# Kernel optimization log

Hardware: AMD Instinct MI355X
Metric: run time of the kernel (lower is better)

The kernel has to match this reference:

```python
import jax, jax.numpy as jnp
import numpy as np

G, N, E, F_IN, F_OUT, C = 256, 512, 4096, 64, 64, 16


def setup_inputs() -> dict:
    key = jax.random.key(0)
    ks = jax.random.split(key, 6)
    x_batch = jax.random.normal(ks[0], (G, N, F_IN), dtype=jnp.float32)
    edge_index_batch = jax.random.randint(ks[1], (G, 2, E), 0, N, dtype=jnp.int32)
    conv_weight = jax.random.normal(ks[2], (F_OUT, F_IN), dtype=jnp.float32) * (1.0 / np.sqrt(F_IN))
    conv_bias = jax.random.normal(ks[3], (F_OUT,), dtype=jnp.float32) * 0.02
    lin_weight = jax.random.normal(ks[4], (C, F_OUT * N), dtype=jnp.float32) * (1.0 / np.sqrt(F_OUT * N))
    lin_bias = jax.random.normal(ks[5], (C,), dtype=jnp.float32) * 0.02
    return {"x_batch": x_batch, "edge_index_batch": edge_index_batch,
            "conv_weight": conv_weight, "conv_bias": conv_bias,
            "lin_weight": lin_weight, "lin_bias": lin_bias}


def _gcn_conv_graph(xw, edge_index, self_loops):
    # xw: [N, F_OUT] (already linearly transformed), edge_index: [2, E]
    row = jnp.concatenate([edge_index[0], self_loops])  # sources
    col = jnp.concatenate([edge_index[1], self_loops])  # targets
    ones = jnp.ones(row.shape[0], dtype=xw.dtype)
    deg = jax.ops.segment_sum(ones, col, num_segments=N)  # degree at target nodes
    dinv = jnp.where(deg > 0, jax.lax.rsqrt(deg), jnp.zeros_like(deg))
    norm = dinv[row] * dinv[col]                          # [E+N]
    msgs = xw[row] * norm[:, None]                        # gather + normalize
    return jax.ops.segment_sum(msgs, col, num_segments=N)  # scatter-add at targets


def reference(x_batch, edge_index_batch, conv_weight, conv_bias, lin_weight, lin_bias):
    # GCNConv (PyG defaults: self-loops, symmetric normalization, post-agg bias)
    xw = jnp.einsum('gnf,of->gno', x_batch, conv_weight)  # [G, N, F_OUT]
    self_loops = jnp.arange(N, dtype=edge_index_batch.dtype)
    h = jax.vmap(_gcn_conv_graph, in_axes=(0, 0, None))(xw, edge_index_batch, self_loops)
    h = h + conv_bias
    h = jax.nn.relu(h)
    flat = h.reshape(h.shape[0], -1)                      # [G, N*F_OUT]
    logits = flat @ lin_weight.T + lin_bias               # [G, C]
    return jax.nn.log_softmax(logits, axis=-1)
```

## Files before the change

kernel.cpp:

```cpp
#include <hip/hip_runtime.h>

#define Gn 256
#define Nn 512
#define En 4096
#define Fn 64
#define Cn 16
#define ET (En + Nn)

typedef _Float16 halfv8 __attribute__((ext_vector_type(8)));
typedef _Float16 halfv4 __attribute__((ext_vector_type(4)));
typedef float    f32x4  __attribute__((ext_vector_type(4)));

__device__ __forceinline__ float pk_norm(unsigned p) {
    return (float)__builtin_bit_cast(_Float16, (unsigned short)(p & 0xffffu));
}

__global__ __launch_bounds__(1024, 4) void gcn_agg_conv(
    const float* __restrict__ x,
    const int*   __restrict__ ei,
    const float* __restrict__ w,
    const float* __restrict__ wbias,
    _Float16* __restrict__ hout)
{
    __shared__ unsigned short xs_h[Nn * Fn];
    __shared__ unsigned short xhs[Nn * Fn];
    __shared__ unsigned short wts[Fn * Fn];
    __shared__ unsigned int   epk[ET + 8];
    __shared__ float dinv[Nn];
    __shared__ int   cnt[Nn];
    __shared__ int   wsum[8];

    const int g    = blockIdx.x;
    const int tid  = threadIdx.x;
    const int lane = tid & 63;
    const int wid  = tid >> 6;

    const float* xg = x + (size_t)g * Nn * Fn;
    const int*   es = ei + (size_t)g * 2 * En;
    const int*   ed = es + En;

    if (tid < Nn) dinv[tid] = 1.0f;
    __syncthreads();

    for (int e = tid; e < En; e += 1024) atomicAdd(&dinv[ed[e]], 1.0f);
    #pragma unroll
    for (int it = 0; it < 8; ++it) {
        int idx = tid + it * 1024;
        float4 v = *(const float4*)(xg + idx * 4);
        halfv4 hv; hv[0]=(_Float16)v.x; hv[1]=(_Float16)v.y;
                   hv[2]=(_Float16)v.z; hv[3]=(_Float16)v.w;
        *(halfv4*)((char*)xs_h + idx * 8) = hv;
    }
    {
        int o = tid >> 4, f0 = (tid & 15) * 4;
        float4 v = *(const float4*)(w + o * Fn + f0);
        halfv4 hv; hv[0]=(_Float16)v.x; hv[1]=(_Float16)v.y;
                   hv[2]=(_Float16)v.z; hv[3]=(_Float16)v.w;
        int blk = f0 >> 3, hf = (f0 >> 2) & 1;
        *(halfv4*)((char*)wts + o * 128 + ((blk ^ (o & 7)) * 16) + hf * 8) = hv;
    }
    __syncthreads();

    int c = 0;
    if (tid < Nn) { float d = dinv[tid]; c = (int)d; dinv[tid] = rsqrtf(d); }
    int v_ = c;
    #pragma unroll
    for (int off = 1; off < 64; off <<= 1) {
        int u = __shfl_up(v_, off, 64);
        if (lane >= off) v_ += u;
    }
    if (wid < 8 && lane == 63) wsum[wid] = v_;
    __syncthreads();
    if (tid == 0) { int a = 0; for (int i = 0; i < 8; ++i) { int t = wsum[i]; wsum[i] = a; a += t; } }
    __syncthreads();
    if (tid < Nn) cnt[tid] = v_ - c + wsum[wid];
    __syncthreads();

    for (int e = tid; e < ET; e += 1024) {
        int s, t;
        if (e < En) { s = es[e]; t = ed[e]; } else { s = e - En; t = s; }
        float nrm = dinv[s] * dinv[t];
        int slot = atomicAdd(&cnt[t], 1);
        unsigned short nb = __builtin_bit_cast(unsigned short, (_Float16)nrm);
        epk[slot] = ((unsigned)s << 16) | nb;
    }
    __syncthreads();

    {
        const int qid = lane >> 4, fl = lane & 15;
        for (int r = 0; r < 8; ++r) {
            int t = r * 64 + wid * 4 + qid;
            int beg = (t == 0) ? 0 : cnt[t - 1];
            int end = cnt[t];
            float a0 = 0.f, a1 = 0.f, a2 = 0.f, a3 = 0.f;
            unsigned pA0 = epk[beg],     pA1 = epk[beg + 1];
            unsigned pA2 = epk[beg + 2], pA3 = epk[beg + 3];
            int j = beg;
            for (; j + 4 <= end; j += 4) {
                unsigned pB0 = epk[j + 4], pB1 = epk[j + 5];
                unsigned pB2 = epk[j + 6], pB3 = epk[j + 7];
                int s0 = pA0 >> 16, s1 = pA1 >> 16, s2 = pA2 >> 16, s3 = pA3 >> 16;
                float n0 = pk_norm(pA0), n1 = pk_norm(pA1);
                float n2 = pk_norm(pA2), n3 = pk_norm(pA3);
                halfv4 x0 = *(const halfv4*)((const char*)xs_h + s0 * 128 + fl * 8);
                halfv4 x1 = *(const halfv4*)((const char*)xs_h + s1 * 128 + fl * 8);
                halfv4 x2 = *(const halfv4*)((const char*)xs_h + s2 * 128 + fl * 8);
                halfv4 x3 = *(const halfv4*)((const char*)xs_h + s3 * 128 + fl * 8);
                a0 += n0 * (float)x0[0] + n1 * (float)x1[0] + n2 * (float)x2[0] + n3 * (float)x3[0];
                a1 += n0 * (float)x0[1] + n1 * (float)x1[1] + n2 * (float)x2[1] + n3 * (float)x3[1];
                a2 += n0 * (float)x0[2] + n1 * (float)x1[2] + n2 * (float)x2[2] + n3 * (float)x3[2];
                a3 += n0 * (float)x0[3] + n1 * (float)x1[3] + n2 * (float)x2[3] + n3 * (float)x3[3];
                pA0 = pB0; pA1 = pB1; pA2 = pB2; pA3 = pB3;
            }
            for (; j < end; ++j) {
                int s = pA0 >> 16;
                float nm = pk_norm(pA0);
                halfv4 xv = *(const halfv4*)((const char*)xs_h + s * 128 + fl * 8);
                a0 += nm * (float)xv[0]; a1 += nm * (float)xv[1];
                a2 += nm * (float)xv[2]; a3 += nm * (float)xv[3];
                pA0 = pA1; pA1 = pA2; pA2 = pA3;
            }
            halfv4 hv; hv[0]=(_Float16)a0; hv[1]=(_Float16)a1;
                       hv[2]=(_Float16)a2; hv[3]=(_Float16)a3;
            int dw = t * 32 + (((fl >> 1) ^ (t & 7)) * 4) + (fl & 1) * 2;
            *(halfv4*)((char*)xhs + dw * 4) = hv;
        }
    }
    __syncthreads();

    {
        const int m = lane & 15, q = lane >> 4;
        #pragma unroll
        for (int j = 0; j < 8; ++j) {
            int idx = wid * 8 + j, tm = idx >> 2, to = idx & 3;
            int n = tm * 16 + m, o = to * 16 + m;
            halfv8 X0 = *(const halfv8*)((const char*)xhs + n * 128 + ((q       ^ (n & 7)) * 16));
            halfv8 X1 = *(const halfv8*)((const char*)xhs + n * 128 + (((4 + q) ^ (n & 7)) * 16));
            halfv8 W0 = *(const halfv8*)((const char*)wts + o * 128 + ((q       ^ (o & 7)) * 16));
            halfv8 W1 = *(const halfv8*)((const char*)wts + o * 128 + (((4 + q) ^ (o & 7)) * 16));
            f32x4 acc = {0.f, 0.f, 0.f, 0.f};
            acc = __builtin_amdgcn_mfma_f32_16x16x32_f16(W0, X0, acc, 0, 0, 0);
            acc = __builtin_amdgcn_mfma_f32_16x16x32_f16(W1, X1, acc, 0, 0, 0);
            float4 bq = *(const float4*)&wbias[to * 16 + q * 4];
            halfv4 hv;
            hv[0] = (_Float16)fmaxf(acc[0] + bq.x, 0.0f);
            hv[1] = (_Float16)fmaxf(acc[1] + bq.y, 0.0f);
            hv[2] = (_Float16)fmaxf(acc[2] + bq.z, 0.0f);
            hv[3] = (_Float16)fmaxf(acc[3] + bq.w, 0.0f);
            int sw = (to * 4 + q) ^ m;
            *(halfv4*)((char*)xs_h + n * 128 + sw * 8) = hv;
        }
    }
    __syncthreads();

    {
        _Float16* hg = hout + (size_t)g * (Nn * Fn);
        #pragma unroll
        for (int it = 0; it < 8; ++it) {
            int i = tid + it * 1024;
            int n = i >> 4, g64 = i & 15;
            uint2 vv = *(const uint2*)((const char*)xs_h + (n * 16 + (g64 ^ (n & 15))) * 8);
            *(uint2*)((char*)hg + (size_t)i * 8) = vv;
        }
    }
}

__global__ __launch_bounds__(256) void gcn_linear(
    const _Float16* __restrict__ h,
    const float* __restrict__ lw,
    float* __restrict__ part)
{
    __shared__ float red[4][64][4];
    const int cx = blockIdx.x;
    const int gy = blockIdx.y;
    const int tid = threadIdx.x, lane = tid & 63, wid = tid >> 6;
    const int ml = lane & 15, q = lane >> 4;

    const size_t kbase = (size_t)cx * 1024 + wid * 256;
    const _Float16* ha = h  + (size_t)(gy * 16 + ml) * (Nn * Fn) + kbase + q * 8;
    const float*    lb = lw + (size_t)ml * (Nn * Fn) + kbase + q * 8;

    f32x4 acc = {0.f, 0.f, 0.f, 0.f};
    #pragma unroll
    for (int ks = 0; ks < 8; ++ks) {
        halfv8 a = *(const halfv8*)(ha + ks * 32);
        float4 b0 = *(const float4*)(lb + ks * 32);
        float4 b1 = *(const float4*)(lb + ks * 32 + 4);
        halfv8 b; b[0]=(_Float16)b0.x; b[1]=(_Float16)b0.y; b[2]=(_Float16)b0.z;
                  b[3]=(_Float16)b0.w; b[4]=(_Float16)b1.x; b[5]=(_Float16)b1.y;
                  b[6]=(_Float16)b1.z; b[7]=(_Float16)b1.w;
        acc = __builtin_amdgcn_mfma_f32_16x16x32_f16(a, b, acc, 0, 0, 0);
    }
    #pragma unroll
    for (int r = 0; r < 4; ++r) red[wid][lane][r] = acc[r];
    __syncthreads();
    {
        int m = tid >> 4, cc = tid & 15;
        int sl = (m >> 2) * 16 + cc, rg = m & 3;
        float v = red[0][sl][rg] + red[1][sl][rg] + red[2][sl][rg] + red[3][sl][rg];
        part[(((size_t)(gy * 16 + m)) * 32 + cx) * Cn + cc] = v;
    }
}

__global__ __launch_bounds__(64) void gcn_softmax(
    const float* __restrict__ part,
    const float* __restrict__ lbias,
    float* __restrict__ out)
{
    const int g = blockIdx.x, lane = threadIdx.x;
    if (lane < Cn) {
        float v = lbias[lane];
        #pragma unroll
        for (int s = 0; s < 32; ++s) v += part[((size_t)g * 32 + s) * Cn + lane];
        float m = v;
        #pragma unroll
        for (int off = 8; off > 0; off >>= 1) m = fmaxf(m, __shfl_xor(m, off, 16));
        float ex = expf(v - m);
        float ssum = ex;
        #pragma unroll
        for (int off = 8; off > 0; off >>= 1) ssum += __shfl_xor(ssum, off, 16);
        out[g * Cn + lane] = v - m - logf(ssum);
    }
}

extern "C" void kernel_launch(void* const* d_in, const int* in_sizes, int n_in,
                              void* d_out, int out_size, void* d_ws, size_t ws_size,
                              hipStream_t stream) {
    const float* x  = (const float*)d_in[0];
    const int*   ei = (const int*)d_in[1];
    const float* w  = (const float*)d_in[2];
    const float* wb = (const float*)d_in[3];
    const float* lw = (const float*)d_in[4];
    const float* lb = (const float*)d_in[5];
    float* out = (float*)d_out;

    _Float16* hbuf = (_Float16*)d_ws;
    float* part = (float*)((char*)d_ws + (size_t)Gn * Nn * Fn * 2);

    hipLaunchKernelGGL(gcn_agg_conv, dim3(Gn), dim3(1024), 0, stream,
                       x, ei, w, wb, hbuf);
    hipLaunchKernelGGL(gcn_linear, dim3(32, 16), dim3(256), 0, stream,
                       hbuf, lw, part);
    hipLaunchKernelGGL(gcn_softmax, dim3(Gn), dim3(64), 0, stream,
                       part, lb, out);
}
```

Baseline: 113.4 us.

## Split fused GCN kernel into conversion, CSR build, half-graph aggregation and linear kernels

Replaces the single per-graph aggregation kernel with separate kernels. One converts x to fp16 in global memory, one converts and permutes the linear weight to fp16, one builds the CSR edge list per graph, and one aggregates half a graph per block with gathers read from global memory instead of LDS. The hidden layer is written in a tiled layout matched to the permuted linear weights, and the linear kernel now loads fp16 weights directly. The aim is more blocks per graph, less LDS per block for higher occupancy, and no repeated weight conversion. In exchange it adds extra launches and global round trips for the converted x and the CSR arrays.

```diff
diff --git a/kernel.cpp b/kernel.cpp
--- a/kernel.cpp
+++ b/kernel.cpp
@@ -6,6 +6,7 @@
 #define Fn 64
 #define Cn 16
 #define ET (En + Nn)
+#define EPAD 4616
 
 typedef _Float16 halfv8 __attribute__((ext_vector_type(8)));
 typedef _Float16 halfv4 __attribute__((ext_vector_type(4)));
@@ -15,97 +16,141 @@
     return (float)__builtin_bit_cast(_Float16, (unsigned short)(p & 0xffffu));
 }
 
-__global__ __launch_bounds__(1024, 4) void gcn_agg_conv(
-    const float* __restrict__ x,
-    const int*   __restrict__ ei,
-    const float* __restrict__ w,
-    const float* __restrict__ wbias,
+__global__ __launch_bounds__(256) void cvt_x(const float* __restrict__ x,
+                                             _Float16* __restrict__ xc) {
+    size_t base = (size_t)blockIdx.x * 256 + threadIdx.x;
+    #pragma unroll
+    for (int it = 0; it < 4; ++it) {
+        size_t i = base + (size_t)it * (2048 * 256);
+        float4 v = ((const float4*)x)[i];
+        halfv4 h; h[0]=(_Float16)v.x; h[1]=(_Float16)v.y;
+                  h[2]=(_Float16)v.z; h[3]=(_Float16)v.w;
+        ((halfv4*)xc)[i] = h;
+    }
+}
+
+__global__ __launch_bounds__(256) void cvt_lw_perm(const float* __restrict__ lw,
+                                                   _Float16* __restrict__ lwh) {
+    int u = blockIdx.x * 256 + threadIdx.x;
+    int c = u >> 13, v = u & 8191;
+    int jobidx = v >> 6, q = (v >> 4) & 3, m = v & 15;
+    int n = (jobidx >> 2) * 16 + m;
+    int o = (jobidx & 3) * 16 + q * 4;
+    float4 f = *(const float4*)(lw + (size_t)c * (Nn * Fn) + n * 64 + o);
+    halfv4 h; h[0]=(_Float16)f.x; h[1]=(_Float16)f.y;
+              h[2]=(_Float16)f.z; h[3]=(_Float16)f.w;
+    *(halfv4*)(lwh + (size_t)c * (Nn * Fn) + (size_t)v * 4) = h;
+}
+
+__global__ __launch_bounds__(256) void build_csr(const int* __restrict__ ei,
+                                                 unsigned* __restrict__ epkG,
+                                                 int* __restrict__ cntG) {
+    __shared__ int      degL[Nn];
+    __shared__ float    dinvL[Nn];
+    __shared__ int      cntE[Nn];
+    __shared__ unsigned epkL[ET];
+    __shared__ int      wsum[4];
+    const int g = blockIdx.x, tid = threadIdx.x;
+    const int lane = tid & 63, wid = tid >> 6;
+    const int* es = ei + (size_t)g * 2 * En;
+    const int* ed = es + En;
+
+    degL[tid] = 0; degL[tid + 256] = 0;
+    __syncthreads();
+    for (int e = tid; e < En; e += 256) atomicAdd(&degL[ed[e]], 1);
+    __syncthreads();
+
+    const int t2 = tid * 2;
+    int cA = degL[t2] + 1, cB = degL[t2 + 1] + 1;
+    dinvL[t2]     = rsqrtf((float)cA);
+    dinvL[t2 + 1] = rsqrtf((float)cB);
+    int p = cA + cB, v = p;
+    #pragma unroll
+    for (int off = 1; off < 64; off <<= 1) {
+        int u = __shfl_up(v, off, 64);
+        if (lane >= off) v += u;
+    }
+    if (lane == 63) wsum[wid] = v;
+    __syncthreads();
+    if (tid == 0) { int a = 0; for (int i = 0; i < 4; ++i) { int t = wsum[i]; wsum[i] = a; a += t; } }
+    __syncthreads();
+    int pe = v - p + wsum[wid];
+    cntE[t2] = pe;
+    cntE[t2 + 1] = pe + cA;
+    __syncthreads();
+
+    for (int e = tid; e < ET; e += 256) {
+        int s, t;
+        if (e < En) { s = es[e]; t = ed[e]; } else { s = t = e - En; }
+        float nrm = dinvL[s] * dinvL[t];
+        int slot = atomicAdd(&cntE[t], 1);
+        unsigned short nb = __builtin_bit_cast(unsigned short, (_Float16)nrm);
+        epkL[slot] = ((unsigned)s << 16) | nb;
+    }
+    __syncthreads();
+
+    for (int i = tid; i < ET; i += 256) epkG[(size_t)g * EPAD + i] = epkL[i];
+    cntG[(size_t)g * Nn + t2]     = cntE[t2];
+    cntG[(size_t)g * Nn + t2 + 1] = cntE[t2 + 1];
+}
+
+__global__ __launch_bounds__(512, 4) void agg_conv(
+    const _Float16* __restrict__ xc,
+    const unsigned* __restrict__ epkG,
+    const int*      __restrict__ cntG,
+    const float*    __restrict__ w,
+    const float*    __restrict__ wbias,
     _Float16* __restrict__ hout)
 {
-    __shared__ unsigned short xs_h[Nn * Fn];
-    __shared__ unsigned short xhs[Nn * Fn];
+    __shared__ unsigned short xhs[256 * Fn];
     __shared__ unsigned short wts[Fn * Fn];
-    __shared__ unsigned int   epk[ET + 8];
-    __shared__ float dinv[Nn];
-    __shared__ int   cnt[Nn];
-    __shared__ int   wsum[8];
-
-    const int g    = blockIdx.x;
-    const int tid  = threadIdx.x;
-    const int lane = tid & 63;
-    const int wid  = tid >> 6;
-
-    const float* xg = x + (size_t)g * Nn * Fn;
-    const int*   es = ei + (size_t)g * 2 * En;
-    const int*   ed = es + En;
-
-    if (tid < Nn) dinv[tid] = 1.0f;
-    __syncthreads();
-
-    for (int e = tid; e < En; e += 1024) atomicAdd(&dinv[ed[e]], 1.0f);
-    #pragma unroll
-    for (int it = 0; it < 8; ++it) {
-        int idx = tid + it * 1024;
-        float4 v = *(const float4*)(xg + idx * 4);
-        halfv4 hv; hv[0]=(_Float16)v.x; hv[1]=(_Float16)v.y;
-                   hv[2]=(_Float16)v.z; hv[3]=(_Float16)v.w;
-        *(halfv4*)((char*)xs_h + idx * 8) = hv;
-    }
-    {
-        int o = tid >> 4, f0 = (tid & 15) * 4;
-        float4 v = *(const float4*)(w + o * Fn + f0);
-        halfv4 hv; hv[0]=(_Float16)v.x; hv[1]=(_Float16)v.y;
-                   hv[2]=(_Float16)v.z; hv[3]=(_Float16)v.w;
-        int blk = f0 >> 3, hf = (f0 >> 2) & 1;
-        *(halfv4*)((char*)wts + o * 128 + ((blk ^ (o & 7)) * 16) + hf * 8) = hv;
-    }
-    __syncthreads();
-
-    int c = 0;
-    if (tid < Nn) { float d = dinv[tid]; c = (int)d; dinv[tid] = rsqrtf(d); }
-    int v_ = c;
-    #pragma unroll
-    for (int off = 1; off < 64; off <<= 1) {
-        int u = __shfl_up(v_, off, 64);
-        if (lane >= off) v_ += u;
-    }
-    if (wid < 8 && lane == 63) wsum[wid] = v_;
-    __syncthreads();
-    if (tid == 0) { int a = 0; for (int i = 0; i < 8; ++i) { int t = wsum[i]; wsum[i] = a; a += t; } }
-    __syncthreads();
-    if (tid < Nn) cnt[tid] = v_ - c + wsum[wid];
-    __syncthreads();
-
-    for (int e = tid; e < ET; e += 1024) {
-        int s, t;
-        if (e < En) { s = es[e]; t = ed[e]; } else { s = e - En; t = s; }
-        float nrm = dinv[s] * dinv[t];
-        int slot = atomicAdd(&cnt[t], 1);
-        unsigned short nb = __builtin_bit_cast(unsigned short, (_Float16)nrm);
-        epk[slot] = ((unsigned)s << 16) | nb;
-    }
-    __syncthreads();
-
-    {
+    __shared__ unsigned epkL[ET + 16];
+    __shared__ int cntl[260];
+    const int hh = blockIdx.x, g = blockIdx.y;
+    const int tid = threadIdx.x, lane = tid & 63, wid = tid >> 6;
+    const int tbase = hh * 256;
+
+    const int slotlo = (hh == 0) ? 0 : cntG[(size_t)g * Nn + tbase - 1];
+    const int slothi = cntG[(size_t)g * Nn + tbase + 255];
+    const int total  = slothi - slotlo;
+
+    if (tid < 257)
+        cntl[tid] = (tid == 0) ? slotlo : cntG[(size_t)g * Nn + tbase + tid - 1];
+    for (int i = tid; i < total; i += 512)
+        epkL[i] = epkG[(size_t)g * EPAD + slotlo + i];
+    {
+        int o = tid >> 3, b8 = tid & 7;
+        float4 va = *(const float4*)(w + o * Fn + b8 * 8);
+        float4 vb = *(const float4*)(w + o * Fn + b8 * 8 + 4);
+        halfv8 hv; hv[0]=(_Float16)va.x; hv[1]=(_Float16)va.y;
+                   hv[2]=(_Float16)va.z; hv[3]=(_Float16)va.w;
+                   hv[4]=(_Float16)vb.x; hv[5]=(_Float16)vb.y;
+                   hv[6]=(_Float16)vb.z; hv[7]=(_Float16)vb.w;
+        *(halfv8*)((char*)wts + o * 128 + ((b8 ^ (o & 7)) * 16)) = hv;
+    }
+    __syncthreads();
+
+    {
+        const _Float16* xgc = xc + (size_t)g * (Nn * Fn);
         const int qid = lane >> 4, fl = lane & 15;
         for (int r = 0; r < 8; ++r) {
-            int t = r * 64 + wid * 4 + qid;
-            int beg = (t == 0) ? 0 : cnt[t - 1];
-            int end = cnt[t];
+            int tl = r * 32 + wid * 4 + qid;
+            int beg = cntl[tl] - slotlo;
+            int end = cntl[tl + 1] - slotlo;
             float a0 = 0.f, a1 = 0.f, a2 = 0.f, a3 = 0.f;
-            unsigned pA0 = epk[beg],     pA1 = epk[beg + 1];
-            unsigned pA2 = epk[beg + 2], pA3 = epk[beg + 3];
+            unsigned pA0 = epkL[beg],     pA1 = epkL[beg + 1];
+            unsigned pA2 = epkL[beg + 2], pA3 = epkL[beg + 3];
             int j = beg;
             for (; j + 4 <= end; j += 4) {
-                unsigned pB0 = epk[j + 4], pB1 = epk[j + 5];
-                unsigned pB2 = epk[j + 6], pB3 = epk[j + 7];
+                unsigned pB0 = epkL[j + 4], pB1 = epkL[j + 5];
+                unsigned pB2 = epkL[j + 6], pB3 = epkL[j + 7];
                 int s0 = pA0 >> 16, s1 = pA1 >> 16, s2 = pA2 >> 16, s3 = pA3 >> 16;
                 float n0 = pk_norm(pA0), n1 = pk_norm(pA1);
                 float n2 = pk_norm(pA2), n3 = pk_norm(pA3);
-                halfv4 x0 = *(const halfv4*)((const char*)xs_h + s0 * 128 + fl * 8);
-                halfv4 x1 = *(const halfv4*)((const char*)xs_h + s1 * 128 + fl * 8);
-                halfv4 x2 = *(const halfv4*)((const char*)xs_h + s2 * 128 + fl * 8);
-                halfv4 x3 = *(const halfv4*)((const char*)xs_h + s3 * 128 + fl * 8);
+                halfv4 x0 = *(const halfv4*)(xgc + s0 * Fn + fl * 4);
+                halfv4 x1 = *(const halfv4*)(xgc + s1 * Fn + fl * 4);
+                halfv4 x2 = *(const halfv4*)(xgc + s2 * Fn + fl * 4);
+                halfv4 x3 = *(const halfv4*)(xgc + s3 * Fn + fl * 4);
                 a0 += n0 * (float)x0[0] + n1 * (float)x1[0] + n2 * (float)x2[0] + n3 * (float)x3[0];
                 a1 += n0 * (float)x0[1] + n1 * (float)x1[1] + n2 * (float)x2[1] + n3 * (float)x3[1];
                 a2 += n0 * (float)x0[2] + n1 * (float)x1[2] + n2 * (float)x2[2] + n3 * (float)x3[2];
@@ -115,14 +160,14 @@
             for (; j < end; ++j) {
                 int s = pA0 >> 16;
                 float nm = pk_norm(pA0);
-                halfv4 xv = *(const halfv4*)((const char*)xs_h + s * 128 + fl * 8);
+                halfv4 xv = *(const halfv4*)(xgc + s * Fn + fl * 4);
                 a0 += nm * (float)xv[0]; a1 += nm * (float)xv[1];
                 a2 += nm * (float)xv[2]; a3 += nm * (float)xv[3];
                 pA0 = pA1; pA1 = pA2; pA2 = pA3;
             }
             halfv4 hv; hv[0]=(_Float16)a0; hv[1]=(_Float16)a1;
                        hv[2]=(_Float16)a2; hv[3]=(_Float16)a3;
-            int dw = t * 32 + (((fl >> 1) ^ (t & 7)) * 4) + (fl & 1) * 2;
+            int dw = tl * 32 + (((fl >> 1) ^ (tl & 7)) * 4) + (fl & 1) * 2;
             *(halfv4*)((char*)xhs + dw * 4) = hv;
         }
     }
@@ -132,8 +177,10 @@
         const int m = lane & 15, q = lane >> 4;
         #pragma unroll
         for (int j = 0; j < 8; ++j) {
-            int idx = wid * 8 + j, tm = idx >> 2, to = idx & 3;
-            int n = tm * 16 + m, o = to * 16 + m;
+            int idx = wid * 8 + j;
+            int tm = idx >> 2, to = idx & 3;
+            int n = tm * 16 + m;
+            int o = to * 16 + m;
             halfv8 X0 = *(const halfv8*)((const char*)xhs + n * 128 + ((q       ^ (n & 7)) * 16));
             halfv8 X1 = *(const halfv8*)((const char*)xhs + n * 128 + (((4 + q) ^ (n & 7)) * 16));
             halfv8 W0 = *(const halfv8*)((const char*)wts + o * 128 + ((q       ^ (o & 7)) * 16));
@@ -147,48 +194,31 @@
             hv[1] = (_Float16)fmaxf(acc[1] + bq.y, 0.0f);
             hv[2] = (_Float16)fmaxf(acc[2] + bq.z, 0.0f);
             hv[3] = (_Float16)fmaxf(acc[3] + bq.w, 0.0f);
-            int sw = (to * 4 + q) ^ m;
-            *(halfv4*)((char*)xs_h + n * 128 + sw * 8) = hv;
+            size_t off = (size_t)g * (Nn * Fn)
+                       + (size_t)(((hh * 16 + tm) * 4 + to) * 256 + lane * 4);
+            *(halfv4*)(hout + off) = hv;
         }
     }
-    __syncthreads();
-
-    {
-        _Float16* hg = hout + (size_t)g * (Nn * Fn);
-        #pragma unroll
-        for (int it = 0; it < 8; ++it) {
-            int i = tid + it * 1024;
-            int n = i >> 4, g64 = i & 15;
-            uint2 vv = *(const uint2*)((const char*)xs_h + (n * 16 + (g64 ^ (n & 15))) * 8);
-            *(uint2*)((char*)hg + (size_t)i * 8) = vv;
-        }
-    }
-}
-
-__global__ __launch_bounds__(256) void gcn_linear(
+}
+
+__global__ __launch_bounds__(256) void linear_mfma(
     const _Float16* __restrict__ h,
-    const float* __restrict__ lw,
+    const _Float16* __restrict__ lwh,
     float* __restrict__ part)
 {
     __shared__ float red[4][64][4];
-    const int cx = blockIdx.x;
-    const int gy = blockIdx.y;
+    const int cx = blockIdx.x, gy = blockIdx.y;
     const int tid = threadIdx.x, lane = tid & 63, wid = tid >> 6;
     const int ml = lane & 15, q = lane >> 4;
-
     const size_t kbase = (size_t)cx * 1024 + wid * 256;
-    const _Float16* ha = h  + (size_t)(gy * 16 + ml) * (Nn * Fn) + kbase + q * 8;
-    const float*    lb = lw + (size_t)ml * (Nn * Fn) + kbase + q * 8;
+    const _Float16* ha = h   + (size_t)(gy * 16 + ml) * (Nn * Fn) + kbase + q * 8;
+    const _Float16* lb = lwh + (size_t)ml * (Nn * Fn) + kbase + q * 8;
 
     f32x4 acc = {0.f, 0.f, 0.f, 0.f};
     #pragma unroll
     for (int ks = 0; ks < 8; ++ks) {
         halfv8 a = *(const halfv8*)(ha + ks * 32);
-        float4 b0 = *(const float4*)(lb + ks * 32);
-        float4 b1 = *(const float4*)(lb + ks * 32 + 4);
-        halfv8 b; b[0]=(_Float16)b0.x; b[1]=(_Float16)b0.y; b[2]=(_Float16)b0.z;
-                  b[3]=(_Float16)b0.w; b[4]=(_Float16)b1.x; b[5]=(_Float16)b1.y;
-                  b[6]=(_Float16)b1.z; b[7]=(_Float16)b1.w;
+        halfv8 b = *(const halfv8*)(lb + ks * 32);
         acc = __builtin_amdgcn_mfma_f32_16x16x32_f16(a, b, acc, 0, 0, 0);
     }
     #pragma unroll
@@ -198,13 +228,12 @@
         int m = tid >> 4, cc = tid & 15;
         int sl = (m >> 2) * 16 + cc, rg = m & 3;
         float v = red[0][sl][rg] + red[1][sl][rg] + red[2][sl][rg] + red[3][sl][rg];
-        part[(((size_t)(gy * 16 + m)) * 32 + cx) * Cn + cc] = v;
+        part[((size_t)(gy * 16 + m) * 32 + cx) * Cn + cc] = v;
     }
 }
 
 __global__ __launch_bounds__(64) void gcn_softmax(
-    const float* __restrict__ part,
-    const float* __restrict__ lbias,
+    const float* __restrict__ part, const float* __restrict__ lbias,
     float* __restrict__ out)
 {
     const int g = blockIdx.x, lane = threadIdx.x;
@@ -234,13 +263,21 @@
     const float* lb = (const float*)d_in[5];
     float* out = (float*)d_out;
 
-    _Float16* hbuf = (_Float16*)d_ws;
-    float* part = (float*)((char*)d_ws + (size_t)Gn * Nn * Fn * 2);
-
-    hipLaunchKernelGGL(gcn_agg_conv, dim3(Gn), dim3(1024), 0, stream,
-                       x, ei, w, wb, hbuf);
-    hipLaunchKernelGGL(gcn_linear, dim3(32, 16), dim3(256), 0, stream,
-                       hbuf, lw, part);
-    hipLaunchKernelGGL(gcn_softmax, dim3(Gn), dim3(64), 0, stream,
+    char* wsp = (char*)d_ws;
+    _Float16* xc   = (_Float16*)(wsp);
+    _Float16* lwh  = (_Float16*)(wsp + 16777216);
+    unsigned* epkG = (unsigned*)(wsp + 17825792);
+    int*      cntG = (int*)     (wsp + 22552576);
+    _Float16* hbuf = (_Float16*)(wsp + 23076864);
+    float*    part = (float*)   (wsp + 39854080);
+
+    hipLaunchKernelGGL(cvt_x,       dim3(2048),    dim3(256), 0, stream, x, xc);
+    hipLaunchKernelGGL(cvt_lw_perm, dim3(512),     dim3(256), 0, stream, lw, lwh);
+    hipLaunchKernelGGL(build_csr,   dim3(Gn),      dim3(256), 0, stream, ei, epkG, cntG);
+    hipLaunchKernelGGL(agg_conv,    dim3(2, Gn),   dim3(512), 0, stream,
+                       xc, epkG, cntG, w, wb, hbuf);
+    hipLaunchKernelGGL(linear_mfma, dim3(32, 16),  dim3(256), 0, stream,
+                       hbuf, lwh, part);
+    hipLaunchKernelGGL(gcn_softmax, dim3(Gn),      dim3(64),  0, stream,
                        part, lb, out);
 }
```

Result: slower. 134.4 us (+18.5%).
